# Performance work log

Hardware: AMD Instinct MI355X
Metric: run time of the kernel (lower is better)

The kernel has to match this reference:

```python
import jax, jax.numpy as jnp
import numpy as np

B = 2048        # graphs
MAX_LEN = 254   # nodes per graph (pad target)
DIM = 64
NF = 78         # num_features_xd
DEG = 8
N = B * MAX_LEN         # 520192 nodes
E = N * DEG             # 4161536 edges
BN_EPS = 1e-5
LN_EPS = 1e-5


def setup_inputs() -> dict:
    key = jax.random.key(0)
    ks = jax.random.split(key, 24)
    x = jax.random.normal(ks[0], (N, NF), jnp.float32)
    # intra-graph random edges: (src, dst) within the same graph
    g = jax.random.randint(ks[1], (E,), 0, B)
    src = g * MAX_LEN + jax.random.randint(ks[2], (E,), 0, MAX_LEN)
    dst = g * MAX_LEN + jax.random.randint(ks[3], (E,), 0, MAX_LEN)
    edge_index = jnp.stack([src, dst]).astype(jnp.int32)
    batch = (jnp.arange(N) // MAX_LEN).astype(jnp.int32)
    batch_len = jnp.full((B,), MAX_LEN, jnp.int32)

    def lin(k, fan_in, shape):
        return jax.random.uniform(k, shape, jnp.float32, -1.0, 1.0) / np.sqrt(fan_in)

    # conv1 MLP: 78->64->64
    w1a = lin(ks[4], NF, (NF, DIM)); b1a = lin(ks[5], NF, (DIM,))
    w1b = lin(ks[6], DIM, (DIM, DIM)); b1b = lin(ks[7], DIM, (DIM,))
    # convs 2-5 stacked: 64->64->64
    Wa = lin(ks[8], DIM, (4, DIM, DIM)); ba = lin(ks[9], DIM, (4, DIM))
    Wb = lin(ks[10], DIM, (4, DIM, DIM)); bb = lin(ks[11], DIM, (4, DIM))
    bn_gamma = jnp.ones((5, DIM), jnp.float32)
    bn_beta = jnp.zeros((5, DIM), jnp.float32)
    fc_w = lin(ks[12], DIM, (DIM, DIM)); fc_b = lin(ks[13], DIM, (DIM,))
    ln_gamma = jnp.ones((DIM,), jnp.float32)
    ln_beta = jnp.zeros((DIM,), jnp.float32)
    return {
        "x": x, "edge_index": edge_index, "batch": batch,
        "batch_len": batch_len, "max_len": MAX_LEN,
        "w1a": w1a, "b1a": b1a, "w1b": w1b, "b1b": b1b,
        "Wa": Wa, "ba": ba, "Wb": Wb, "bb": bb,
        "bn_gamma": bn_gamma, "bn_beta": bn_beta,
        "fc_w": fc_w, "fc_b": fc_b,
        "ln_gamma": ln_gamma, "ln_beta": ln_beta,
    }


def _gin_layer(h, src, dst, n, W1, b1, W2, b2, gamma, beta):
    # GINConv (eps=0): z_i = MLP(x_i + sum_{j->i} x_j), then ReLU, then BatchNorm (batch stats)
    agg = jax.ops.segment_sum(h[src], dst, num_segments=n)
    z = h + agg
    z = jnp.maximum(z @ W1 + b1, 0.0) @ W2 + b2
    z = jnp.maximum(z, 0.0)
    mean = z.mean(axis=0)
    var = jnp.square(z - mean).mean(axis=0)  # biased var, as torch BN training
    return (z - mean) * jax.lax.rsqrt(var + BN_EPS) * gamma + beta


def reference(x, edge_index, batch, batch_len, max_len,
              w1a, b1a, w1b, b1b, Wa, ba, Wb, bb,
              bn_gamma, bn_beta, fc_w, fc_b, ln_gamma, ln_beta):
    n = x.shape[0]
    src, dst = edge_index[0], edge_index[1]
    h = _gin_layer(x, src, dst, n, w1a, b1a, w1b, b1b, bn_gamma[0], bn_beta[0])
    for i in range(4):
        h = _gin_layer(h, src, dst, n, Wa[i], ba[i], Wb[i], bb[i],
                       bn_gamma[i + 1], bn_beta[i + 1])
    # get_nodes_att_f: pad per-graph node features to [B, max_len, dim]
    nb = batch_len.shape[0]
    offsets = jnp.cumsum(batch_len) - batch_len            # start index of each graph
    pos = jnp.arange(n, dtype=jnp.int32) - offsets[batch]  # node position within graph
    x_seq = jnp.zeros((nb, max_len, h.shape[1]), h.dtype).at[batch, pos].set(h)
    # global_add_pool + fc + relu + (dropout eval: identity) + layernorm
    pooled = jax.ops.segment_sum(h, batch, num_segments=nb)
    y = jnp.maximum(pooled @ fc_w + fc_b, 0.0)
    mu = y.mean(axis=-1, keepdims=True)
    var = jnp.square(y - mu).mean(axis=-1, keepdims=True)
    y = (y - mu) * jax.lax.rsqrt(var + LN_EPS) * ln_gamma + ln_beta
    return (x_seq, y)
```

## Files before the change

### kernel.cpp

```cpp
#include <hip/hip_runtime.h>

#define NGRAPH 2048
#define MAXLEN 254
#define NNODE 520192
#define NEDGE 4161536
#define NF 78
#define CAP 32
#define BN_EPS 1e-5f
#define LN_EPS 1e-5f

__global__ __launch_bounds__(256) void k_init(int* __restrict__ deg, float* __restrict__ stats) {
    int i = blockIdx.x * 256 + threadIdx.x;
    deg[i] = 0;
    if (blockIdx.x == 0) {
        for (int j = threadIdx.x; j < 5 * 128; j += 256) stats[j] = 0.f;
    }
}

__global__ __launch_bounds__(256) void k_build(const int* __restrict__ ei,
                                               int* __restrict__ deg,
                                               unsigned char* __restrict__ elist) {
    int e = blockIdx.x * 256 + threadIdx.x;
    int s = ei[e];
    int d = ei[NEDGE + e];
    int g = d / MAXLEN;
    int r = atomicAdd(&deg[d], 1);
    elist[(size_t)d * CAP + r] = (unsigned char)(s - g * MAXLEN);
}

__global__ __launch_bounds__(256) void k_gemm78(const float* __restrict__ x,
                                                const float* __restrict__ W,
                                                float* __restrict__ out) {
    __shared__ float sW[NF * 64];
    for (int i = threadIdx.x; i < NF * 64; i += 256) sW[i] = W[i];
    __syncthreads();
    int node = blockIdx.x * 256 + threadIdx.x;
    const float* xr = x + (size_t)node * NF;
    float a[64];
#pragma unroll
    for (int c = 0; c < 64; c++) a[c] = 0.f;
    for (int k2 = 0; k2 < NF / 2; k2++) {
        float2 xv = ((const float2*)xr)[k2];
        const float* w0 = sW + (2 * k2) * 64;
#pragma unroll
        for (int c = 0; c < 64; c++) a[c] += xv.x * w0[c];
#pragma unroll
        for (int c = 0; c < 64; c++) a[c] += xv.y * w0[64 + c];
    }
    float* orow = out + ((size_t)node << 6);
#pragma unroll
    for (int c = 0; c < 64; c += 4)
        *(float4*)(orow + c) = make_float4(a[c], a[c + 1], a[c + 2], a[c + 3]);
}

__device__ __forceinline__ void second_matmul(const float (&a)[64], const float* __restrict__ sW2,
                                              const float* __restrict__ sb2,
                                              float* __restrict__ orow) {
#pragma unroll
    for (int cb = 0; cb < 64; cb += 16) {
        float o[16];
#pragma unroll
        for (int j = 0; j < 16; j++) o[j] = sb2[cb + j];
#pragma unroll
        for (int k = 0; k < 64; k++) {
            float ak = a[k];
#pragma unroll
            for (int j = 0; j < 16; j++) o[j] += ak * sW2[k * 64 + cb + j];
        }
#pragma unroll
        for (int j = 0; j < 16; j += 4)
            *(float4*)(orow + cb + j) =
                make_float4(fmaxf(o[j], 0.f), fmaxf(o[j + 1], 0.f),
                            fmaxf(o[j + 2], 0.f), fmaxf(o[j + 3], 0.f));
    }
}

template <int FIRST, int FOLD>
__global__ __launch_bounds__(256, 2) void k_layer(const float* __restrict__ hin,
                                                  const unsigned char* __restrict__ elist,
                                                  const int* __restrict__ deg,
                                                  const float* __restrict__ stats,
                                                  const float* __restrict__ gamma,
                                                  const float* __restrict__ beta,
                                                  const float* __restrict__ W1,
                                                  const float* __restrict__ b1,
                                                  const float* __restrict__ W2,
                                                  const float* __restrict__ b2,
                                                  float* __restrict__ hout) {
    __shared__ float sW1[FIRST ? 1 : 64 * 64];
    __shared__ float sW2[64 * 64];
    __shared__ float sb1[64], sb2[64];
    __shared__ float ssc[64], sbi[64];
    if (!FIRST)
        for (int i = threadIdx.x; i < 64 * 64; i += 256) sW1[i] = W1[i];
    for (int i = threadIdx.x; i < 64 * 64; i += 256) sW2[i] = W2[i];
    if (threadIdx.x < 64) {
        sb1[threadIdx.x] = b1[threadIdx.x];
        sb2[threadIdx.x] = b2[threadIdx.x];
        if (FOLD) {
            const float invN = 1.0f / NNODE;
            int c = threadIdx.x;
            float mean = stats[c] * invN;
            float var = stats[64 + c] * invN - mean * mean;
            float sc = gamma[c] * rsqrtf(var + BN_EPS);
            ssc[c] = sc;
            sbi[c] = beta[c] - mean * sc;
        }
    }
    __syncthreads();

    int lb = (int)(blockIdx.x & 7) * 254 + (int)(blockIdx.x >> 3);
    int node = lb * 256 + threadIdx.x;
    int dg = deg[node];
    int base = (node / MAXLEN) * MAXLEN;

    float g[64];
    const float* hr = hin + ((size_t)node << 6);
#pragma unroll
    for (int c4 = 0; c4 < 16; c4++) {
        float4 v = ((const float4*)hr)[c4];
        g[4 * c4] = v.x; g[4 * c4 + 1] = v.y; g[4 * c4 + 2] = v.z; g[4 * c4 + 3] = v.w;
    }
    const unsigned* row = (const unsigned*)(elist + (size_t)node * CAP);
    int ne4 = (dg + 3) >> 2;
    for (int e4 = 0; e4 < ne4; e4++) {
        unsigned pk = row[e4];
#pragma unroll
        for (int j = 0; j < 4; j++) {
            if (4 * e4 + j < dg) {
                const float* sr = hin + ((size_t)(base + (int)((pk >> (8 * j)) & 255u)) << 6);
#pragma unroll
                for (int c4 = 0; c4 < 16; c4++) {
                    float4 v = ((const float4*)sr)[c4];
                    g[4 * c4] += v.x; g[4 * c4 + 1] += v.y;
                    g[4 * c4 + 2] += v.z; g[4 * c4 + 3] += v.w;
                }
            }
        }
    }
    if (FOLD) {
        float kk = (float)(1 + dg);
#pragma unroll
        for (int c = 0; c < 64; c++) g[c] = g[c] * ssc[c] + kk * sbi[c];
    }

    float a[64];
    if (FIRST) {
#pragma unroll
        for (int c = 0; c < 64; c++) a[c] = fmaxf(g[c] + sb1[c], 0.f);
    } else {
#pragma unroll
        for (int c = 0; c < 64; c++) a[c] = sb1[c];
#pragma unroll
        for (int k4 = 0; k4 < 16; k4++) {
            const float* w = sW1 + k4 * 256;
            float g0 = g[4 * k4], g1 = g[4 * k4 + 1], g2 = g[4 * k4 + 2], g3 = g[4 * k4 + 3];
#pragma unroll
            for (int c = 0; c < 64; c++) a[c] += g0 * w[c];
#pragma unroll
            for (int c = 0; c < 64; c++) a[c] += g1 * w[64 + c];
#pragma unroll
            for (int c = 0; c < 64; c++) a[c] += g2 * w[128 + c];
#pragma unroll
            for (int c = 0; c < 64; c++) a[c] += g3 * w[192 + c];
        }
#pragma unroll
        for (int c = 0; c < 64; c++) a[c] = fmaxf(a[c], 0.f);
    }
    second_matmul(a, sW2, sb2, hout + ((size_t)node << 6));
}

__global__ __launch_bounds__(256) void k_bnstats(const float* __restrict__ h,
                                                 float* __restrict__ stats) {
    __shared__ float ss[128];
    if (threadIdx.x < 128) ss[threadIdx.x] = 0.f;
    __syncthreads();
    int tid = blockIdx.x * 256 + threadIdx.x;
    int c4 = (tid & 15) * 4;
    float s0 = 0, s1 = 0, s2 = 0, s3 = 0, q0 = 0, q1 = 0, q2 = 0, q3 = 0;
    const float4* p = (const float4*)h;
    for (size_t i = tid; i < (size_t)NNODE * 16; i += 65536) {
        float4 v = p[i];
        s0 += v.x; q0 += v.x * v.x;
        s1 += v.y; q1 += v.y * v.y;
        s2 += v.z; q2 += v.z * v.z;
        s3 += v.w; q3 += v.w * v.w;
    }
    atomicAdd(&ss[c4], s0);      atomicAdd(&ss[c4 + 1], s1);
    atomicAdd(&ss[c4 + 2], s2);  atomicAdd(&ss[c4 + 3], s3);
    atomicAdd(&ss[64 + c4], q0); atomicAdd(&ss[64 + c4 + 1], q1);
    atomicAdd(&ss[64 + c4 + 2], q2); atomicAdd(&ss[64 + c4 + 3], q3);
    __syncthreads();
    if (threadIdx.x < 128) atomicAdd(&stats[threadIdx.x], ss[threadIdx.x]);
}

__global__ __launch_bounds__(256) void k_final(float* __restrict__ h,
                                               const float* __restrict__ stats,
                                               const float* __restrict__ gamma,
                                               const float* __restrict__ beta,
                                               const float* __restrict__ fcw,
                                               const float* __restrict__ fcb,
                                               const float* __restrict__ lng,
                                               const float* __restrict__ lnb,
                                               float* __restrict__ y) {
    int b = blockIdx.x;
    int q = threadIdx.x >> 6;
    int c = threadIdx.x & 63;
    __shared__ float ssc[64], sbi[64];
    if (threadIdx.x < 64) {
        const float invN = 1.0f / NNODE;
        float mean = stats[c] * invN;
        float var = stats[64 + c] * invN - mean * mean;
        float sc = gamma[c] * rsqrtf(var + BN_EPS);
        ssc[c] = sc;
        sbi[c] = beta[c] - mean * sc;
    }
    __syncthreads();
    float* base = h + (size_t)b * MAXLEN * 64;
    float sc = ssc[c], bi = sbi[c];
    float s = 0.f;
    for (int p = q; p < MAXLEN; p += 4) {
        float v = base[p * 64 + c] * sc + bi;
        base[p * 64 + c] = v;
        s += v;
    }
    __shared__ float sp[4][64];
    sp[q][c] = s;
    __syncthreads();
    __shared__ float pooled[64];
    if (threadIdx.x < 64) pooled[c] = sp[0][c] + sp[1][c] + sp[2][c] + sp[3][c];
    __syncthreads();
    if (threadIdx.x < 64) {
        float accv = fcb[c];
        for (int k = 0; k < 64; k++) accv += pooled[k] * fcw[k * 64 + c];
        accv = fmaxf(accv, 0.f);
        float t = accv;
        for (int o = 32; o; o >>= 1) t += __shfl_xor(t, o, 64);
        float mu = t * (1.0f / 64.0f);
        float d = accv - mu;
        float t2 = d * d;
        for (int o = 32; o; o >>= 1) t2 += __shfl_xor(t2, o, 64);
        float var = t2 * (1.0f / 64.0f);
        y[(size_t)b * 64 + c] = d * rsqrtf(var + LN_EPS) * lng[c] + lnb[c];
    }
}

extern "C" void kernel_launch(void* const* d_in, const int* in_sizes, int n_in,
                              void* d_out, int out_size, void* d_ws, size_t ws_size,
                              hipStream_t stream) {
    const float* x   = (const float*)d_in[0];
    const int*   ei  = (const int*)d_in[1];
    const float* w1a = (const float*)d_in[5];
    const float* b1a = (const float*)d_in[6];
    const float* w1b = (const float*)d_in[7];
    const float* b1b = (const float*)d_in[8];
    const float* Wa  = (const float*)d_in[9];
    const float* ba  = (const float*)d_in[10];
    const float* Wb  = (const float*)d_in[11];
    const float* bb  = (const float*)d_in[12];
    const float* bng = (const float*)d_in[13];
    const float* bnb = (const float*)d_in[14];
    const float* fcw = (const float*)d_in[15];
    const float* fcb = (const float*)d_in[16];
    const float* lng = (const float*)d_in[17];
    const float* lnb = (const float*)d_in[18];

    float* h   = (float*)d_out;
    float* y   = h + (size_t)NNODE * 64;
    float* acc = (float*)d_ws;
    float* stats = acc + (size_t)NNODE * 64;
    int* deg = (int*)(stats + 5 * 128);
    unsigned char* elist = (unsigned char*)(deg + NNODE);

    const int NB_NODE = NNODE / 256;
    const int NB_EDGE = NEDGE / 256;
    (void)in_sizes; (void)n_in; (void)out_size; (void)ws_size;

    k_init<<<NB_NODE, 256, 0, stream>>>(deg, stats);
    k_build<<<NB_EDGE, 256, 0, stream>>>(ei, deg, elist);

    k_gemm78<<<NB_NODE, 256, 0, stream>>>(x, w1a, acc);
    k_layer<1, 0><<<NB_NODE, 256, 0, stream>>>(acc, elist, deg, nullptr, nullptr, nullptr,
                                               nullptr, b1a, w1b, b1b, h);
    k_bnstats<<<256, 256, 0, stream>>>(h, stats);

    for (int L = 1; L <= 4; L++) {
        const float* in = (L & 1) ? h : acc;
        float* out      = (L & 1) ? acc : h;
        k_layer<0, 1><<<NB_NODE, 256, 0, stream>>>(in, elist, deg,
                                                   stats + (L - 1) * 128,
                                                   bng + (size_t)(L - 1) * 64,
                                                   bnb + (size_t)(L - 1) * 64,
                                                   Wa + (size_t)(L - 1) * 4096,
                                                   ba + (size_t)(L - 1) * 64,
                                                   Wb + (size_t)(L - 1) * 4096,
                                                   bb + (size_t)(L - 1) * 64, out);
        k_bnstats<<<256, 256, 0, stream>>>(out, stats + L * 128);
    }

    k_final<<<NGRAPH, 256, 0, stream>>>(h, stats + 4 * 128, bng + 4 * 64, bnb + 4 * 64,
                                        fcw, fcb, lng, lnb, y);
}
```

Baseline: 2.413 ms.

## Read MLP weights directly from global memory and keep accumulators in float4 registers

The layer kernel no longer stages W1, W2 and the biases in shared memory. Every thread now reads the weights straight from global memory as uniform float4 loads, which may become scalar/constant loads served from cache. Accumulators and gathered features are held in explicitly named float4 registers built with macros, so the arrays stay in registers and the neighbour-index word is prefetched one iteration ahead. This removes the LDS fill and most LDS reads, and the block sync in the first layer. In exchange it relies on the compiler keeping weight loads uniform and cached, and register pressure may rise.

Result: slower. 2.638 ms (+9.3%).

```diff
diff --git a/kernel.cpp b/kernel.cpp
--- a/kernel.cpp
+++ b/kernel.cpp
@@ -8,6 +8,11 @@
 #define CAP 32
 #define BN_EPS 1e-5f
 #define LN_EPS 1e-5f
+
+#define REP16A(F) F(0) F(1) F(2) F(3) F(4) F(5) F(6) F(7) \
+                  F(8) F(9) F(10) F(11) F(12) F(13) F(14) F(15)
+#define REP16B(F) F(0) F(1) F(2) F(3) F(4) F(5) F(6) F(7) \
+                  F(8) F(9) F(10) F(11) F(12) F(13) F(14) F(15)
 
 __global__ __launch_bounds__(256) void k_init(int* __restrict__ deg, float* __restrict__ stats) {
     int i = blockIdx.x * 256 + threadIdx.x;
@@ -53,29 +58,7 @@
         *(float4*)(orow + c) = make_float4(a[c], a[c + 1], a[c + 2], a[c + 3]);
 }
 
-__device__ __forceinline__ void second_matmul(const float (&a)[64], const float* __restrict__ sW2,
-                                              const float* __restrict__ sb2,
-                                              float* __restrict__ orow) {
-#pragma unroll
-    for (int cb = 0; cb < 64; cb += 16) {
-        float o[16];
-#pragma unroll
-        for (int j = 0; j < 16; j++) o[j] = sb2[cb + j];
-#pragma unroll
-        for (int k = 0; k < 64; k++) {
-            float ak = a[k];
-#pragma unroll
-            for (int j = 0; j < 16; j++) o[j] += ak * sW2[k * 64 + cb + j];
-        }
-#pragma unroll
-        for (int j = 0; j < 16; j += 4)
-            *(float4*)(orow + cb + j) =
-                make_float4(fmaxf(o[j], 0.f), fmaxf(o[j + 1], 0.f),
-                            fmaxf(o[j + 2], 0.f), fmaxf(o[j + 3], 0.f));
-    }
-}
-
-template <int FIRST, int FOLD>
+template <int FIRST>
 __global__ __launch_bounds__(256, 2) void k_layer(const float* __restrict__ hin,
                                                   const unsigned char* __restrict__ elist,
                                                   const int* __restrict__ deg,
@@ -87,87 +70,99 @@
                                                   const float* __restrict__ W2,
                                                   const float* __restrict__ b2,
                                                   float* __restrict__ hout) {
-    __shared__ float sW1[FIRST ? 1 : 64 * 64];
-    __shared__ float sW2[64 * 64];
-    __shared__ float sb1[64], sb2[64];
     __shared__ float ssc[64], sbi[64];
-    if (!FIRST)
-        for (int i = threadIdx.x; i < 64 * 64; i += 256) sW1[i] = W1[i];
-    for (int i = threadIdx.x; i < 64 * 64; i += 256) sW2[i] = W2[i];
-    if (threadIdx.x < 64) {
-        sb1[threadIdx.x] = b1[threadIdx.x];
-        sb2[threadIdx.x] = b2[threadIdx.x];
-        if (FOLD) {
+    if constexpr (!FIRST) {
+        if (threadIdx.x < 64) {
+            int c = threadIdx.x;
             const float invN = 1.0f / NNODE;
-            int c = threadIdx.x;
             float mean = stats[c] * invN;
             float var = stats[64 + c] * invN - mean * mean;
             float sc = gamma[c] * rsqrtf(var + BN_EPS);
             ssc[c] = sc;
             sbi[c] = beta[c] - mean * sc;
         }
-    }
-    __syncthreads();
+        __syncthreads();
+    }
 
     int lb = (int)(blockIdx.x & 7) * 254 + (int)(blockIdx.x >> 3);
     int node = lb * 256 + threadIdx.x;
     int dg = deg[node];
     int base = (node / MAXLEN) * MAXLEN;
 
-    float g[64];
-    const float* hr = hin + ((size_t)node << 6);
-#pragma unroll
-    for (int c4 = 0; c4 < 16; c4++) {
-        float4 v = ((const float4*)hr)[c4];
-        g[4 * c4] = v.x; g[4 * c4 + 1] = v.y; g[4 * c4 + 2] = v.z; g[4 * c4 + 3] = v.w;
-    }
-    const unsigned* row = (const unsigned*)(elist + (size_t)node * CAP);
+#define DECLG(i) float4 g##i;
+    REP16A(DECLG)
+    const float4* hr4 = (const float4*)(hin + ((size_t)node << 6));
+#define LOADG(i) g##i = hr4[i];
+    REP16A(LOADG)
+    const unsigned* rowu = (const unsigned*)(elist + (size_t)node * CAP);
     int ne4 = (dg + 3) >> 2;
+    unsigned pk = rowu[0];
     for (int e4 = 0; e4 < ne4; e4++) {
-        unsigned pk = row[e4];
+        unsigned nxt = rowu[e4 + 1];
 #pragma unroll
         for (int j = 0; j < 4; j++) {
             if (4 * e4 + j < dg) {
-                const float* sr = hin + ((size_t)(base + (int)((pk >> (8 * j)) & 255u)) << 6);
-#pragma unroll
-                for (int c4 = 0; c4 < 16; c4++) {
-                    float4 v = ((const float4*)sr)[c4];
-                    g[4 * c4] += v.x; g[4 * c4 + 1] += v.y;
-                    g[4 * c4 + 2] += v.z; g[4 * c4 + 3] += v.w;
-                }
+                const float4* sr4 =
+                    (const float4*)(hin + ((size_t)(base + (int)((pk >> (8 * j)) & 255u)) << 6));
+#define ADDG(i) { float4 v_ = sr4[i]; g##i.x += v_.x; g##i.y += v_.y; \
+                  g##i.z += v_.z; g##i.w += v_.w; }
+                REP16A(ADDG)
             }
         }
-    }
-    if (FOLD) {
-        float kk = (float)(1 + dg);
-#pragma unroll
-        for (int c = 0; c < 64; c++) g[c] = g[c] * ssc[c] + kk * sbi[c];
-    }
-
-    float a[64];
-    if (FIRST) {
-#pragma unroll
-        for (int c = 0; c < 64; c++) a[c] = fmaxf(g[c] + sb1[c], 0.f);
+        pk = nxt;
+    }
+    float kk = (float)(1 + dg);
+    if constexpr (!FIRST) {
+#define BNG(i) { const float4 s_ = *(const float4*)(ssc + 4 * (i)); \
+                 const float4 b_ = *(const float4*)(sbi + 4 * (i)); \
+                 g##i.x = g##i.x * s_.x + kk * b_.x; g##i.y = g##i.y * s_.y + kk * b_.y; \
+                 g##i.z = g##i.z * s_.z + kk * b_.z; g##i.w = g##i.w * s_.w + kk * b_.w; }
+        REP16A(BNG)
+    }
+
+#define DECLA(i) float4 a##i;
+    REP16A(DECLA)
+    const float4* b1q = (const float4*)b1;
+    if constexpr (FIRST) {
+#define AFROMG(i) { float4 b_ = b1q[i]; a##i.x = fmaxf(g##i.x + b_.x, 0.f); \
+                    a##i.y = fmaxf(g##i.y + b_.y, 0.f); a##i.z = fmaxf(g##i.z + b_.z, 0.f); \
+                    a##i.w = fmaxf(g##i.w + b_.w, 0.f); }
+        REP16A(AFROMG)
     } else {
-#pragma unroll
-        for (int c = 0; c < 64; c++) a[c] = sb1[c];
-#pragma unroll
-        for (int k4 = 0; k4 < 16; k4++) {
-            const float* w = sW1 + k4 * 256;
-            float g0 = g[4 * k4], g1 = g[4 * k4 + 1], g2 = g[4 * k4 + 2], g3 = g[4 * k4 + 3];
-#pragma unroll
-            for (int c = 0; c < 64; c++) a[c] += g0 * w[c];
-#pragma unroll
-            for (int c = 0; c < 64; c++) a[c] += g1 * w[64 + c];
-#pragma unroll
-            for (int c = 0; c < 64; c++) a[c] += g2 * w[128 + c];
-#pragma unroll
-            for (int c = 0; c < 64; c++) a[c] += g3 * w[192 + c];
-        }
-#pragma unroll
-        for (int c = 0; c < 64; c++) a[c] = fmaxf(a[c], 0.f);
-    }
-    second_matmul(a, sW2, sb2, hout + ((size_t)node << 6));
+#define AINIT(i) a##i = b1q[i];
+        REP16A(AINIT)
+        const float4* W1q = (const float4*)W1;
+#define AFMA(i) { float4 w_ = w4_[i]; a##i.x += ak_ * w_.x; a##i.y += ak_ * w_.y; \
+                  a##i.z += ak_ * w_.z; a##i.w += ak_ * w_.w; }
+#define MLP1K(K4) { const float4 r_ = g##K4; const float4* wb_ = W1q + (K4) * 64; \
+    { const float ak_ = r_.x; const float4* w4_ = wb_;      REP16B(AFMA) } \
+    { const float ak_ = r_.y; const float4* w4_ = wb_ + 16; REP16B(AFMA) } \
+    { const float ak_ = r_.z; const float4* w4_ = wb_ + 32; REP16B(AFMA) } \
+    { const float ak_ = r_.w; const float4* w4_ = wb_ + 48; REP16B(AFMA) } }
+        REP16A(MLP1K)
+#define RELUA(i) a##i.x = fmaxf(a##i.x, 0.f); a##i.y = fmaxf(a##i.y, 0.f); \
+                 a##i.z = fmaxf(a##i.z, 0.f); a##i.w = fmaxf(a##i.w, 0.f);
+        REP16A(RELUA)
+    }
+
+#define DECLO(i) float4 o##i;
+    REP16A(DECLO)
+    const float4* b2q = (const float4*)b2;
+#define OINIT(i) o##i = b2q[i];
+    REP16A(OINIT)
+    const float4* W2q = (const float4*)W2;
+#define OFMA(i) { float4 w_ = w4_[i]; o##i.x += ak_ * w_.x; o##i.y += ak_ * w_.y; \
+                  o##i.z += ak_ * w_.z; o##i.w += ak_ * w_.w; }
+#define MLP2K(K4) { const float4 r_ = a##K4; const float4* wb_ = W2q + (K4) * 64; \
+    { const float ak_ = r_.x; const float4* w4_ = wb_;      REP16B(OFMA) } \
+    { const float ak_ = r_.y; const float4* w4_ = wb_ + 16; REP16B(OFMA) } \
+    { const float ak_ = r_.z; const float4* w4_ = wb_ + 32; REP16B(OFMA) } \
+    { const float ak_ = r_.w; const float4* w4_ = wb_ + 48; REP16B(OFMA) } }
+    REP16A(MLP2K)
+    float4* out4 = (float4*)(hout + ((size_t)node << 6));
+#define STOREO(i) out4[i] = make_float4(fmaxf(o##i.x, 0.f), fmaxf(o##i.y, 0.f), \
+                                        fmaxf(o##i.z, 0.f), fmaxf(o##i.w, 0.f));
+    REP16A(STOREO)
 }
 
 __global__ __launch_bounds__(256) void k_bnstats(const float* __restrict__ h,
@@ -280,22 +275,22 @@
     k_build<<<NB_EDGE, 256, 0, stream>>>(ei, deg, elist);
 
     k_gemm78<<<NB_NODE, 256, 0, stream>>>(x, w1a, acc);
-    k_layer<1, 0><<<NB_NODE, 256, 0, stream>>>(acc, elist, deg, nullptr, nullptr, nullptr,
-                                               nullptr, b1a, w1b, b1b, h);
+    k_layer<1><<<NB_NODE, 256, 0, stream>>>(acc, elist, deg, nullptr, nullptr, nullptr,
+                                            nullptr, b1a, w1b, b1b, h);
     k_bnstats<<<256, 256, 0, stream>>>(h, stats);
 
     for (int L = 1; L <= 4; L++) {
         const float* in = (L & 1) ? h : acc;
         float* out      = (L & 1) ? acc : h;
-        k_layer<0, 1><<<NB_NODE, 256, 0, stream>>>(in, elist, deg,
-                                                   stats + (L - 1) * 128,
-                                                   bng + (size_t)(L - 1) * 64,
-                                                   bnb + (size_t)(L - 1) * 64,
-                                                   Wa + (size_t)(L - 1) * 4096,
-                                                   ba + (size_t)(L - 1) * 64,
-                                                   Wb + (size_t)(L - 1) * 4096,
-                                                   bb + (size_t)(L - 1) * 64, out);
-        k_bnstats<<<256, 256, 0, stream>>>(out, stats + L * 128);
+        k_layer<0><<<NB_NODE, 256, 0, stream>>>(in, elist, deg,
+                                                stats + (size_t)(L - 1) * 128,
+                                                bng + (size_t)(L - 1) * 64,
+                                                bnb + (size_t)(L - 1) * 64,
+                                                Wa + (size_t)(L - 1) * 4096,
+                                                ba + (size_t)(L - 1) * 64,
+                                                Wb + (size_t)(L - 1) * 4096,
+                                                bb + (size_t)(L - 1) * 64, out);
+        k_bnstats<<<256, 256, 0, stream>>>(out, stats + (size_t)L * 128);
     }
 
     k_final<<<NGRAPH, 256, 0, stream>>>(h, stats + 4 * 128, bng + 4 * 64, bnb + 4 * 64,
```
